# Performance work log

Hardware: AMD Instinct MI355X
Metric: run time of the kernel (lower is better)

## Reference

```python
import jax, jax.numpy as jnp
import numpy as np

B, L, T = 256, 256, 50  # batch, max_len, num_tags


def setup_inputs() -> dict:
    key = jax.random.key(0)
    k1, k2, k3 = jax.random.split(key, 3)
    feats = jax.random.normal(k1, (B, L, T), dtype=jnp.float32)
    trans_m = jax.random.normal(k2, (T, T), dtype=jnp.float32)
    tags = jax.random.randint(k3, (B, L), 0, T)
    mask = jnp.ones((B, L), dtype=jnp.int32)
    return {"feats": feats, "trans_m": trans_m, "tags": tags, "mask": mask}


def _normalizer(logits, trans_m, m):
    # logits: (L, B, T), m: (L, B) float mask
    alpha0 = logits[0]  # (B, T)

    def step(alpha, inp):
        emit, mt = inp  # (B, T), (B,)
        # (B, T_from, T_to) broadcast add, logsumexp over T_from
        tmp = alpha[:, :, None] + trans_m[None, :, :] + emit[:, None, :]
        new = jax.nn.logsumexp(tmp, axis=1)
        alpha = jnp.where(mt[:, None] > 0, new, alpha)
        return alpha, None

    alpha, _ = jax.lax.scan(step, alpha0, (logits[1:], m[1:]))
    return jax.nn.logsumexp(alpha, axis=1)  # (B,)


def _gold_score(logits, trans_m, tags_t, m):
    # logits: (L, B, T); tags_t: (L, B); m: (L, B)
    trans_sc = trans_m[tags_t[:-1], tags_t[1:]] * m[1:]  # (L-1, B)
    emit_sc = jnp.take_along_axis(logits, tags_t[:, :, None], axis=2)[..., 0] * m  # (L, B)
    return jnp.sum(trans_sc + emit_sc[:-1], axis=0) + emit_sc[-1]  # (B,)


def reference(feats, trans_m, tags, mask):
    # feats: (B, L, T) -> (L, B, T); include_start_end_trans=False
    logits = jnp.transpose(feats, (1, 0, 2))
    tags_t = tags.T
    m = mask.T.astype(feats.dtype)
    all_path = _normalizer(logits, trans_m, m)
    gold = _gold_score(logits, trans_m, tags_t, m)
    return all_path - gold  # (B,) loss per example
```

## Files before the change

### kernel.cpp

```cpp
#include <hip/hip_runtime.h>
#include <math.h>


#define TAGS 50
#define LEN 256
#define NB 256
#define HALF 128
#define INV_LN2 1.4426950408889634f
#define LN2 0.6931471805599453f

typedef __attribute__((ext_vector_type(8))) short bf16x8;
typedef __attribute__((ext_vector_type(4))) float f32x4;

#if __has_builtin(__builtin_amdgcn_exp2f)
#define EXP2F(x) __builtin_amdgcn_exp2f(x)
#else
#define EXP2F(x) exp2f(x)
#endif
#if __has_builtin(__builtin_amdgcn_logf)
#define LOG2F(x) __builtin_amdgcn_logf(x)
#else
#define LOG2F(x) log2f(x)
#endif
#if __has_builtin(__builtin_amdgcn_rcpf)
#define RCPF(x) __builtin_amdgcn_rcpf(x)
#else
#define RCPF(x) (1.0f / (x))
#endif

__device__ __forceinline__ float readlane_f(float v, int srclane) {
  return __builtin_bit_cast(float,
      __builtin_amdgcn_readlane(__builtin_bit_cast(int, v), srclane));
}

__device__ __forceinline__ int bf16pair(float lo, float hi) {
  unsigned lb = (__builtin_bit_cast(unsigned, lo) + 0x8000u) >> 16;
  unsigned hb = (__builtin_bit_cast(unsigned, hi) + 0x8000u) & 0xFFFF0000u;
  return (int)(hb | lb);
}

union U8 { int i[4]; bf16x8 v; };

#define WS_U(b)  ((b) * 64)
#define WS_W(b)  ((NB + (b)) * 64)
#define WS_SF(b) (2 * NB * 64 + (b))
#define WS_SB(b) (2 * NB * 64 + NB + (b))

__global__ __launch_bounds__(64) void crf_scan_kernel(
    const float* __restrict__ feats,
    const float* __restrict__ trans,
    const int*   __restrict__ mask,
    float*       __restrict__ ws)
{
  const int bid    = blockIdx.x;
  const bool is_fwd = bid < NB;
  const int b      = is_fwd ? bid : bid - NB;
  const int lane   = threadIdx.x;
  const int q      = lane >> 4;
  const int n      = lane & 15;

  __shared__ __align__(16) float fl[HALF * TAGS];
  __shared__ int ml[HALF];

  const int base_l = is_fwd ? 0 : HALF;
  const float* fb = feats + ((size_t)b * LEN + base_l) * TAGS;
  const int*   mb = mask + b * LEN + base_l;

  {
    const float4* fv = (const float4*)fb;
    for (int i = lane; i < (HALF * TAGS) / 4; i += 64) {
      float4 v4 = fv[i];
      v4.x *= INV_LN2; v4.y *= INV_LN2; v4.z *= INV_LN2; v4.w *= INV_LN2;
      *(float4*)&fl[i * 4] = v4;
    }
    for (int i = lane; i < HALF; i += 64) ml[i] = mb[i];
  }

  int tcl[4], vld[4];
#pragma unroll
  for (int t = 0; t < 4; ++t) {
    const int tg = n + 16 * t;
    vld[t] = tg < TAGS;
    tcl[t] = vld[t] ? tg : (TAGS - 1);
  }

  U8 Bfr[4][2];
#pragma unroll
  for (int t = 0; t < 4; ++t)
#pragma unroll
    for (int c = 0; c < 2; ++c)
#pragma unroll
      for (int r = 0; r < 4; ++r) {
        const int col = 16 * t + n;
        const int tag0 = 16 * c + 4 * q + r;
        const int tag1 = tag0 + 32;
        float e0 = 0.0f, e1 = 0.0f;
        if (col < TAGS) {
          if (tag0 < TAGS)
            e0 = EXP2F((is_fwd ? trans[tag0 * TAGS + col]
                               : trans[col * TAGS + tag0]) * INV_LN2);
          if (tag1 < TAGS)
            e1 = EXP2F((is_fwd ? trans[tag1 * TAGS + col]
                               : trans[col * TAGS + tag1]) * INV_LN2);
        }
        Bfr[t][c].i[r] = bf16pair(e0, e1);
      }

  int addr[4];
#pragma unroll
  for (int r = 0; r < 4; ++r) addr[r] = (4 * q + r) * 4;

  __syncthreads();

  const f32x4 zero4 = {0.0f, 0.0f, 0.0f, 0.0f};
  float v[4], S;

  if (is_fwd) {
    const float c0 = fl[0];
#pragma unroll
    for (int t = 0; t < 4; ++t) v[t] = vld[t] ? EXP2F(fl[tcl[t]] - c0) : 0.0f;
    S = c0;

    float eh[4];
#pragma unroll
    for (int t = 0; t < 4; ++t) eh[t] = EXP2F(fl[TAGS + tcl[t]]);
    int m_nxt = ml[1];

    for (int l = 1; l < HALF; ++l) {
      const int m_cur = m_nxt;
      const int ln = (l + 1 < HALF) ? (l + 1) : (HALF - 1);

      const int P0 = bf16pair(v[0], v[2]);
      const int P1 = bf16pair(v[1], v[3]);
      const float cc = readlane_f(v[0], 0);
      const float rr = RCPF(cc);

      U8 A0, A1;
#pragma unroll
      for (int r = 0; r < 4; ++r) {
        A0.i[r] = __builtin_amdgcn_ds_bpermute(addr[r], P0);
        A1.i[r] = __builtin_amdgcn_ds_bpermute(addr[r], P1);
      }

      f32x4 d0 = __builtin_amdgcn_mfma_f32_16x16x32_bf16(A0.v, Bfr[0][0].v, zero4, 0, 0, 0);
      f32x4 d1 = __builtin_amdgcn_mfma_f32_16x16x32_bf16(A0.v, Bfr[1][0].v, zero4, 0, 0, 0);
      f32x4 d2 = __builtin_amdgcn_mfma_f32_16x16x32_bf16(A0.v, Bfr[2][0].v, zero4, 0, 0, 0);
      f32x4 d3 = __builtin_amdgcn_mfma_f32_16x16x32_bf16(A0.v, Bfr[3][0].v, zero4, 0, 0, 0);
      f32x4 g0 = __builtin_amdgcn_mfma_f32_16x16x32_bf16(A1.v, Bfr[0][1].v, zero4, 0, 0, 0);
      f32x4 g1 = __builtin_amdgcn_mfma_f32_16x16x32_bf16(A1.v, Bfr[1][1].v, zero4, 0, 0, 0);
      f32x4 g2 = __builtin_amdgcn_mfma_f32_16x16x32_bf16(A1.v, Bfr[2][1].v, zero4, 0, 0, 0);
      f32x4 g3 = __builtin_amdgcn_mfma_f32_16x16x32_bf16(A1.v, Bfr[3][1].v, zero4, 0, 0, 0);

      float ehn[4];
#pragma unroll
      for (int t = 0; t < 4; ++t) ehn[t] = fl[ln * TAGS + tcl[t]];
      const int m_n2 = ml[ln];

      v[0] = ((m_cur > 0) ? (d0[0] + g0[0]) * eh[0] : v[0]) * rr;
      v[1] = ((m_cur > 0) ? (d1[0] + g1[0]) * eh[1] : v[1]) * rr;
      v[2] = ((m_cur > 0) ? (d2[0] + g2[0]) * eh[2] : v[2]) * rr;
      v[3] = ((m_cur > 0) ? (d3[0] + g3[0]) * eh[3] : v[3]) * rr;
      S += LOG2F(cc);
#pragma unroll
      for (int t = 0; t < 4; ++t) eh[t] = EXP2F(ehn[t]);
      m_nxt = m_n2;
    }

    if (lane < 16) {
#pragma unroll
      for (int t = 0; t < 4; ++t) ws[WS_U(b) + n + 16 * t] = v[t];
    }
    if (lane == 0) ws[WS_SF(b)] = S;
  } else {
#pragma unroll
    for (int t = 0; t < 4; ++t) v[t] = vld[t] ? 1.0f : 0.0f;
    S = 0.0f;

    float eh[4];
#pragma unroll
    for (int t = 0; t < 4; ++t) eh[t] = EXP2F(fl[(HALF - 1) * TAGS + tcl[t]]);
    int m_nxt = ml[HALF - 1];

    for (int l = HALF - 1; l >= 0; --l) {
      const int m_cur = m_nxt;
      const int ln = (l > 0) ? (l - 1) : 0;

      const float x0 = v[0] * eh[0];
      const float x1 = v[1] * eh[1];
      const float x2 = v[2] * eh[2];
      const float x3 = v[3] * eh[3];
      const int P0 = bf16pair(x0, x2);
      const int P1 = bf16pair(x1, x3);
      const float cc = readlane_f(v[0], 0);
      const float rr = RCPF(cc);

      U8 A0, A1;
#pragma unroll
      for (int r = 0; r < 4; ++r) {
        A0.i[r] = __builtin_amdgcn_ds_bpermute(addr[r], P0);
        A1.i[r] = __builtin_amdgcn_ds_bpermute(addr[r], P1);
      }

      f32x4 d0 = __builtin_amdgcn_mfma_f32_16x16x32_bf16(A0.v, Bfr[0][0].v, zero4, 0, 0, 0);
      f32x4 d1 = __builtin_amdgcn_mfma_f32_16x16x32_bf16(A0.v, Bfr[1][0].v, zero4, 0, 0, 0);
      f32x4 d2 = __builtin_amdgcn_mfma_f32_16x16x32_bf16(A0.v, Bfr[2][0].v, zero4, 0, 0, 0);
      f32x4 d3 = __builtin_amdgcn_mfma_f32_16x16x32_bf16(A0.v, Bfr[3][0].v, zero4, 0, 0, 0);
      f32x4 g0 = __builtin_amdgcn_mfma_f32_16x16x32_bf16(A1.v, Bfr[0][1].v, zero4, 0, 0, 0);
      f32x4 g1 = __builtin_amdgcn_mfma_f32_16x16x32_bf16(A1.v, Bfr[1][1].v, zero4, 0, 0, 0);
      f32x4 g2 = __builtin_amdgcn_mfma_f32_16x16x32_bf16(A1.v, Bfr[2][1].v, zero4, 0, 0, 0);
      f32x4 g3 = __builtin_amdgcn_mfma_f32_16x16x32_bf16(A1.v, Bfr[3][1].v, zero4, 0, 0, 0);

      float ehn[4];
#pragma unroll
      for (int t = 0; t < 4; ++t) ehn[t] = fl[ln * TAGS + tcl[t]];
      const int m_n2 = ml[ln];

      v[0] = ((m_cur > 0) ? (d0[0] + g0[0]) : v[0]) * rr;
      v[1] = ((m_cur > 0) ? (d1[0] + g1[0]) : v[1]) * rr;
      v[2] = ((m_cur > 0) ? (d2[0] + g2[0]) : v[2]) * rr;
      v[3] = ((m_cur > 0) ? (d3[0] + g3[0]) : v[3]) * rr;
      S += LOG2F(cc);
#pragma unroll
      for (int t = 0; t < 4; ++t) eh[t] = EXP2F(ehn[t]);
      m_nxt = m_n2;
    }

    if (lane < 16) {
#pragma unroll
      for (int t = 0; t < 4; ++t) ws[WS_W(b) + n + 16 * t] = v[t];
    }
    if (lane == 0) ws[WS_SB(b)] = S;
  }
}

__global__ __launch_bounds__(64) void crf_combine_kernel(
    const float* __restrict__ feats,
    const float* __restrict__ trans,
    const int*   __restrict__ tags,
    const int*   __restrict__ mask,
    const float* __restrict__ ws,
    float*       __restrict__ out)
{
  const int b = blockIdx.x;
  const int lane = threadIdx.x;

  float s = ws[WS_U(b) + lane] * ws[WS_W(b) + lane];
#pragma unroll
  for (int off = 32; off; off >>= 1) s += __shfl_xor(s, off, 64);

  const float* fb = feats + (size_t)b * (LEN * TAGS);
  const int*   tb = tags + b * LEN;
  const int*   mb = mask + b * LEN;
  float gp = 0.0f;
#pragma unroll
  for (int k = 0; k < 4; ++k) {
    const int p = lane + 64 * k;
    const int tg = tb[p];
    if (mb[p] > 0) {
      float vv = fb[p * TAGS + tg];
      if (p >= 1) vv += trans[tb[p - 1] * TAGS + tg];
      gp += vv;
    }
  }
#pragma unroll
  for (int off = 32; off; off >>= 1) gp += __shfl_xor(gp, off, 64);

  if (lane == 0) {
    const float Sf = ws[WS_SF(b)];
    const float Sb = ws[WS_SB(b)];
    out[b] = LN2 * (Sf + Sb + LOG2F(s)) - gp;
  }
}

extern "C" void kernel_launch(void* const* d_in, const int* in_sizes, int n_in,
                              void* d_out, int out_size, void* d_ws, size_t ws_size,
                              hipStream_t stream) {
  const float* feats = (const float*)d_in[0];
  const float* trans = (const float*)d_in[1];
  const int*   tags  = (const int*)d_in[2];
  const int*   mask  = (const int*)d_in[3];
  float* out = (float*)d_out;
  float* ws  = (float*)d_ws;

  crf_scan_kernel<<<2 * NB, 64, 0, stream>>>(feats, trans, mask, ws);
  crf_combine_kernel<<<NB, 64, 0, stream>>>(feats, trans, tags, mask, ws, out);
}
```

Baseline: 103.9 us.

## Split sequence into chunks with parallel transfer-matrix products combined afterwards

The sequential forward/backward halves shrink from 128 steps each to 32. The 192 middle steps are split into 6 chunks, and separate blocks compute a 64x64 transfer-matrix product for each chunk with MFMA. The combine kernel chains the chunk matrices as matrix-vector products before the final dot product. This shortens the serial dependency chain per block at the cost of much more MFMA work per step, 6x more blocks, and a large workspace of chunk matrices written and reread. A perm-based bf16 pack replaces the shift/mask pack.

```diff
diff --git a/kernel.cpp b/kernel.cpp
--- a/kernel.cpp
+++ b/kernel.cpp
@@ -5,7 +5,9 @@
 #define TAGS 50
 #define LEN 256
 #define NB 256
-#define HALF 128
+#define VST 32
+#define NCH 6
+#define CST 32
 #define INV_LN2 1.4426950408889634f
 #define LN2 0.6931471805599453f
 
@@ -33,18 +35,24 @@
       __builtin_amdgcn_readlane(__builtin_bit_cast(int, v), srclane));
 }
 
-__device__ __forceinline__ int bf16pair(float lo, float hi) {
-  unsigned lb = (__builtin_bit_cast(unsigned, lo) + 0x8000u) >> 16;
-  unsigned hb = (__builtin_bit_cast(unsigned, hi) + 0x8000u) & 0xFFFF0000u;
-  return (int)(hb | lb);
+__device__ __forceinline__ int bfpack(float lo, float hi) {
+  unsigned lb = __builtin_bit_cast(unsigned, lo) + 0x8000u;
+  unsigned hb = __builtin_bit_cast(unsigned, hi) + 0x8000u;
+#if __has_builtin(__builtin_amdgcn_perm)
+  return (int)__builtin_amdgcn_perm(hb, lb, 0x07060302u);
+#else
+  return (int)((hb & 0xFFFF0000u) | (lb >> 16));
+#endif
 }
 
 union U8 { int i[4]; bf16x8 v; };
 
-#define WS_U(b)  ((b) * 64)
-#define WS_W(b)  ((NB + (b)) * 64)
-#define WS_SF(b) (2 * NB * 64 + (b))
-#define WS_SB(b) (2 * NB * 64 + NB + (b))
+#define WS_U(b)    ((b) * 64)
+#define WS_W(b)    ((NB + (b)) * 64)
+#define WS_SF(b)   (2 * NB * 64 + (b))
+#define WS_SB(b)   (2 * NB * 64 + NB + (b))
+#define WS_SC(b,c) (2 * NB * 64 + 2 * NB + (b) * NCH + (c))
+#define WS_T(b,c)  (2 * NB * 64 + 2 * NB + NB * NCH + (((b) * NCH + (c)) * 64) * 64)
 
 __global__ __launch_bounds__(64) void crf_scan_kernel(
     const float* __restrict__ feats,
@@ -52,184 +60,280 @@
     const int*   __restrict__ mask,
     float*       __restrict__ ws)
 {
-  const int bid    = blockIdx.x;
-  const bool is_fwd = bid < NB;
-  const int b      = is_fwd ? bid : bid - NB;
-  const int lane   = threadIdx.x;
-  const int q      = lane >> 4;
-  const int n      = lane & 15;
-
-  __shared__ __align__(16) float fl[HALF * TAGS];
-  __shared__ int ml[HALF];
-
-  const int base_l = is_fwd ? 0 : HALF;
-  const float* fb = feats + ((size_t)b * LEN + base_l) * TAGS;
-  const int*   mb = mask + b * LEN + base_l;
+  const int bid  = blockIdx.x;
+  const int lane = threadIdx.x;
+  const int q    = lane >> 4;
+  const int n    = lane & 15;
+  const f32x4 zero4 = {0.0f, 0.0f, 0.0f, 0.0f};
+
+  if (bid < 2 * NB) {
+    const bool is_fwd = bid < NB;
+    const int b = is_fwd ? bid : bid - NB;
+
+    __shared__ __align__(16) float fl[VST * TAGS];
+    __shared__ int ml[VST];
+
+    const int base_l = is_fwd ? 0 : (LEN - VST);
+    const float* fb = feats + ((size_t)b * LEN + base_l) * TAGS;
+    const int*   mb = mask + b * LEN + base_l;
+
+    {
+      const float4* fv = (const float4*)fb;
+      for (int i = lane; i < (VST * TAGS) / 4; i += 64) {
+        float4 v4 = fv[i];
+        v4.x *= INV_LN2; v4.y *= INV_LN2; v4.z *= INV_LN2; v4.w *= INV_LN2;
+        *(float4*)&fl[i * 4] = v4;
+      }
+      for (int i = lane; i < VST; i += 64) ml[i] = mb[i];
+    }
+
+    int tcl[4], vld[4];
+#pragma unroll
+    for (int t = 0; t < 4; ++t) {
+      const int tg = n + 16 * t;
+      vld[t] = tg < TAGS;
+      tcl[t] = vld[t] ? tg : (TAGS - 1);
+    }
+
+    U8 Bfr[4][2];
+#pragma unroll
+    for (int t = 0; t < 4; ++t)
+#pragma unroll
+      for (int c = 0; c < 2; ++c)
+#pragma unroll
+        for (int r = 0; r < 4; ++r) {
+          const int col = 16 * t + n;
+          const int tag0 = 16 * c + 4 * q + r;
+          const int tag1 = tag0 + 32;
+          float e0 = 0.0f, e1 = 0.0f;
+          if (col < TAGS) {
+            if (tag0 < TAGS)
+              e0 = EXP2F((is_fwd ? trans[tag0 * TAGS + col]
+                                 : trans[col * TAGS + tag0]) * INV_LN2);
+            if (tag1 < TAGS)
+              e1 = EXP2F((is_fwd ? trans[tag1 * TAGS + col]
+                                 : trans[col * TAGS + tag1]) * INV_LN2);
+          }
+          Bfr[t][c].i[r] = bfpack(e0, e1);
+        }
+
+    int addr[4];
+#pragma unroll
+    for (int r = 0; r < 4; ++r) addr[r] = (4 * q + r) * 4;
+
+    __syncthreads();
+
+    float v[4], S;
+    if (is_fwd) {
+      const float c0 = fl[0];
+#pragma unroll
+      for (int t = 0; t < 4; ++t) v[t] = vld[t] ? EXP2F(fl[tcl[t]] - c0) : 0.0f;
+      S = c0;
+      float eh[4];
+#pragma unroll
+      for (int t = 0; t < 4; ++t) eh[t] = EXP2F(fl[TAGS + tcl[t]]);
+      int m_nxt = ml[1];
+
+      for (int l = 1; l < VST; ++l) {
+        const int m_cur = m_nxt;
+        const int ln = (l + 1 < VST) ? (l + 1) : (VST - 1);
+        const int P0 = bfpack(v[0], v[2]);
+        const int P1 = bfpack(v[1], v[3]);
+        const float cc = readlane_f(v[0], 0);
+        const float rr = RCPF(cc);
+        U8 A0, A1;
+#pragma unroll
+        for (int r = 0; r < 4; ++r) {
+          A0.i[r] = __builtin_amdgcn_ds_bpermute(addr[r], P0);
+          A1.i[r] = __builtin_amdgcn_ds_bpermute(addr[r], P1);
+        }
+        f32x4 d0 = __builtin_amdgcn_mfma_f32_16x16x32_bf16(A0.v, Bfr[0][0].v, zero4, 0, 0, 0);
+        f32x4 d1 = __builtin_amdgcn_mfma_f32_16x16x32_bf16(A0.v, Bfr[1][0].v, zero4, 0, 0, 0);
+        f32x4 d2 = __builtin_amdgcn_mfma_f32_16x16x32_bf16(A0.v, Bfr[2][0].v, zero4, 0, 0, 0);
+        f32x4 d3 = __builtin_amdgcn_mfma_f32_16x16x32_bf16(A0.v, Bfr[3][0].v, zero4, 0, 0, 0);
+        f32x4 g0 = __builtin_amdgcn_mfma_f32_16x16x32_bf16(A1.v, Bfr[0][1].v, zero4, 0, 0, 0);
+        f32x4 g1 = __builtin_amdgcn_mfma_f32_16x16x32_bf16(A1.v, Bfr[1][1].v, zero4, 0, 0, 0);
+        f32x4 g2 = __builtin_amdgcn_mfma_f32_16x16x32_bf16(A1.v, Bfr[2][1].v, zero4, 0, 0, 0);
+        f32x4 g3 = __builtin_amdgcn_mfma_f32_16x16x32_bf16(A1.v, Bfr[3][1].v, zero4, 0, 0, 0);
+        float ehn[4];
+#pragma unroll
+        for (int t = 0; t < 4; ++t) ehn[t] = fl[ln * TAGS + tcl[t]];
+        const int m_n2 = ml[ln];
+        v[0] = ((m_cur > 0) ? (d0[0] + g0[0]) * eh[0] : v[0]) * rr;
+        v[1] = ((m_cur > 0) ? (d1[0] + g1[0]) * eh[1] : v[1]) * rr;
+        v[2] = ((m_cur > 0) ? (d2[0] + g2[0]) * eh[2] : v[2]) * rr;
+        v[3] = ((m_cur > 0) ? (d3[0] + g3[0]) * eh[3] : v[3]) * rr;
+        S += LOG2F(cc);
+#pragma unroll
+        for (int t = 0; t < 4; ++t) eh[t] = EXP2F(ehn[t]);
+        m_nxt = m_n2;
+      }
+      if (lane < 16) {
+#pragma unroll
+        for (int t = 0; t < 4; ++t) ws[WS_U(b) + n + 16 * t] = v[t];
+      }
+      if (lane == 0) ws[WS_SF(b)] = S;
+    } else {
+#pragma unroll
+      for (int t = 0; t < 4; ++t) v[t] = vld[t] ? 1.0f : 0.0f;
+      S = 0.0f;
+      float eh[4];
+#pragma unroll
+      for (int t = 0; t < 4; ++t) eh[t] = EXP2F(fl[(VST - 1) * TAGS + tcl[t]]);
+      int m_nxt = ml[VST - 1];
+
+      for (int l = VST - 1; l >= 0; --l) {
+        const int m_cur = m_nxt;
+        const int ln = (l > 0) ? (l - 1) : 0;
+        const float x0 = v[0] * eh[0];
+        const float x1 = v[1] * eh[1];
+        const float x2 = v[2] * eh[2];
+        const float x3 = v[3] * eh[3];
+        const int P0 = bfpack(x0, x2);
+        const int P1 = bfpack(x1, x3);
+        const float cc = readlane_f(v[0], 0);
+        const float rr = RCPF(cc);
+        U8 A0, A1;
+#pragma unroll
+        for (int r = 0; r < 4; ++r) {
+          A0.i[r] = __builtin_amdgcn_ds_bpermute(addr[r], P0);
+          A1.i[r] = __builtin_amdgcn_ds_bpermute(addr[r], P1);
+        }
+        f32x4 d0 = __builtin_amdgcn_mfma_f32_16x16x32_bf16(A0.v, Bfr[0][0].v, zero4, 0, 0, 0);
+        f32x4 d1 = __builtin_amdgcn_mfma_f32_16x16x32_bf16(A0.v, Bfr[1][0].v, zero4, 0, 0, 0);
+        f32x4 d2 = __builtin_amdgcn_mfma_f32_16x16x32_bf16(A0.v, Bfr[2][0].v, zero4, 0, 0, 0);
+        f32x4 d3 = __builtin_amdgcn_mfma_f32_16x16x32_bf16(A0.v, Bfr[3][0].v, zero4, 0, 0, 0);
+        f32x4 g0 = __builtin_amdgcn_mfma_f32_16x16x32_bf16(A1.v, Bfr[0][1].v, zero4, 0, 0, 0);
+        f32x4 g1 = __builtin_amdgcn_mfma_f32_16x16x32_bf16(A1.v, Bfr[1][1].v, zero4, 0, 0, 0);
+        f32x4 g2 = __builtin_amdgcn_mfma_f32_16x16x32_bf16(A1.v, Bfr[2][1].v, zero4, 0, 0, 0);
+        f32x4 g3 = __builtin_amdgcn_mfma_f32_16x16x32_bf16(A1.v, Bfr[3][1].v, zero4, 0, 0, 0);
+        float ehn[4];
+#pragma unroll
+        for (int t = 0; t < 4; ++t) ehn[t] = fl[ln * TAGS + tcl[t]];
+        const int m_n2 = ml[ln];
+        v[0] = ((m_cur > 0) ? (d0[0] + g0[0]) : v[0]) * rr;
+        v[1] = ((m_cur > 0) ? (d1[0] + g1[0]) : v[1]) * rr;
+        v[2] = ((m_cur > 0) ? (d2[0] + g2[0]) : v[2]) * rr;
+        v[3] = ((m_cur > 0) ? (d3[0] + g3[0]) : v[3]) * rr;
+        S += LOG2F(cc);
+#pragma unroll
+        for (int t = 0; t < 4; ++t) eh[t] = EXP2F(ehn[t]);
+        m_nxt = m_n2;
+      }
+      if (lane < 16) {
+#pragma unroll
+        for (int t = 0; t < 4; ++t) ws[WS_W(b) + n + 16 * t] = v[t];
+      }
+      if (lane == 0) ws[WS_SB(b)] = S;
+    }
+    return;
+  }
 
   {
-    const float4* fv = (const float4*)fb;
-    for (int i = lane; i < (HALF * TAGS) / 4; i += 64) {
-      float4 v4 = fv[i];
-      v4.x *= INV_LN2; v4.y *= INV_LN2; v4.z *= INV_LN2; v4.w *= INV_LN2;
-      *(float4*)&fl[i * 4] = v4;
-    }
-    for (int i = lane; i < HALF; i += 64) ml[i] = mb[i];
-  }
-
-  int tcl[4], vld[4];
-#pragma unroll
-  for (int t = 0; t < 4; ++t) {
-    const int tg = n + 16 * t;
-    vld[t] = tg < TAGS;
-    tcl[t] = vld[t] ? tg : (TAGS - 1);
-  }
-
-  U8 Bfr[4][2];
-#pragma unroll
-  for (int t = 0; t < 4; ++t)
-#pragma unroll
-    for (int c = 0; c < 2; ++c)
-#pragma unroll
-      for (int r = 0; r < 4; ++r) {
-        const int col = 16 * t + n;
-        const int tag0 = 16 * c + 4 * q + r;
-        const int tag1 = tag0 + 32;
-        float e0 = 0.0f, e1 = 0.0f;
-        if (col < TAGS) {
-          if (tag0 < TAGS)
-            e0 = EXP2F((is_fwd ? trans[tag0 * TAGS + col]
-                               : trans[col * TAGS + tag0]) * INV_LN2);
-          if (tag1 < TAGS)
-            e1 = EXP2F((is_fwd ? trans[tag1 * TAGS + col]
-                               : trans[col * TAGS + tag1]) * INV_LN2);
-        }
-        Bfr[t][c].i[r] = bf16pair(e0, e1);
-      }
-
-  int addr[4];
-#pragma unroll
-  for (int r = 0; r < 4; ++r) addr[r] = (4 * q + r) * 4;
-
-  __syncthreads();
-
-  const f32x4 zero4 = {0.0f, 0.0f, 0.0f, 0.0f};
-  float v[4], S;
-
-  if (is_fwd) {
-    const float c0 = fl[0];
-#pragma unroll
-    for (int t = 0; t < 4; ++t) v[t] = vld[t] ? EXP2F(fl[tcl[t]] - c0) : 0.0f;
-    S = c0;
-
-    float eh[4];
-#pragma unroll
-    for (int t = 0; t < 4; ++t) eh[t] = EXP2F(fl[TAGS + tcl[t]]);
-    int m_nxt = ml[1];
-
-    for (int l = 1; l < HALF; ++l) {
-      const int m_cur = m_nxt;
-      const int ln = (l + 1 < HALF) ? (l + 1) : (HALF - 1);
-
-      const int P0 = bf16pair(v[0], v[2]);
-      const int P1 = bf16pair(v[1], v[3]);
-      const float cc = readlane_f(v[0], 0);
-      const float rr = RCPF(cc);
-
-      U8 A0, A1;
-#pragma unroll
-      for (int r = 0; r < 4; ++r) {
-        A0.i[r] = __builtin_amdgcn_ds_bpermute(addr[r], P0);
-        A1.i[r] = __builtin_amdgcn_ds_bpermute(addr[r], P1);
-      }
-
-      f32x4 d0 = __builtin_amdgcn_mfma_f32_16x16x32_bf16(A0.v, Bfr[0][0].v, zero4, 0, 0, 0);
-      f32x4 d1 = __builtin_amdgcn_mfma_f32_16x16x32_bf16(A0.v, Bfr[1][0].v, zero4, 0, 0, 0);
-      f32x4 d2 = __builtin_amdgcn_mfma_f32_16x16x32_bf16(A0.v, Bfr[2][0].v, zero4, 0, 0, 0);
-      f32x4 d3 = __builtin_amdgcn_mfma_f32_16x16x32_bf16(A0.v, Bfr[3][0].v, zero4, 0, 0, 0);
-      f32x4 g0 = __builtin_amdgcn_mfma_f32_16x16x32_bf16(A1.v, Bfr[0][1].v, zero4, 0, 0, 0);
-      f32x4 g1 = __builtin_amdgcn_mfma_f32_16x16x32_bf16(A1.v, Bfr[1][1].v, zero4, 0, 0, 0);
-      f32x4 g2 = __builtin_amdgcn_mfma_f32_16x16x32_bf16(A1.v, Bfr[2][1].v, zero4, 0, 0, 0);
-      f32x4 g3 = __builtin_amdgcn_mfma_f32_16x16x32_bf16(A1.v, Bfr[3][1].v, zero4, 0, 0, 0);
-
-      float ehn[4];
-#pragma unroll
-      for (int t = 0; t < 4; ++t) ehn[t] = fl[ln * TAGS + tcl[t]];
-      const int m_n2 = ml[ln];
-
-      v[0] = ((m_cur > 0) ? (d0[0] + g0[0]) * eh[0] : v[0]) * rr;
-      v[1] = ((m_cur > 0) ? (d1[0] + g1[0]) * eh[1] : v[1]) * rr;
-      v[2] = ((m_cur > 0) ? (d2[0] + g2[0]) * eh[2] : v[2]) * rr;
-      v[3] = ((m_cur > 0) ? (d3[0] + g3[0]) * eh[3] : v[3]) * rr;
-      S += LOG2F(cc);
-#pragma unroll
-      for (int t = 0; t < 4; ++t) eh[t] = EXP2F(ehn[t]);
-      m_nxt = m_n2;
-    }
-
-    if (lane < 16) {
-#pragma unroll
-      for (int t = 0; t < 4; ++t) ws[WS_U(b) + n + 16 * t] = v[t];
-    }
-    if (lane == 0) ws[WS_SF(b)] = S;
-  } else {
-#pragma unroll
-    for (int t = 0; t < 4; ++t) v[t] = vld[t] ? 1.0f : 0.0f;
-    S = 0.0f;
-
-    float eh[4];
-#pragma unroll
-    for (int t = 0; t < 4; ++t) eh[t] = EXP2F(fl[(HALF - 1) * TAGS + tcl[t]]);
-    int m_nxt = ml[HALF - 1];
-
-    for (int l = HALF - 1; l >= 0; --l) {
-      const int m_cur = m_nxt;
-      const int ln = (l > 0) ? (l - 1) : 0;
-
-      const float x0 = v[0] * eh[0];
-      const float x1 = v[1] * eh[1];
-      const float x2 = v[2] * eh[2];
-      const float x3 = v[3] * eh[3];
-      const int P0 = bf16pair(x0, x2);
-      const int P1 = bf16pair(x1, x3);
-      const float cc = readlane_f(v[0], 0);
-      const float rr = RCPF(cc);
-
-      U8 A0, A1;
-#pragma unroll
-      for (int r = 0; r < 4; ++r) {
-        A0.i[r] = __builtin_amdgcn_ds_bpermute(addr[r], P0);
-        A1.i[r] = __builtin_amdgcn_ds_bpermute(addr[r], P1);
-      }
-
-      f32x4 d0 = __builtin_amdgcn_mfma_f32_16x16x32_bf16(A0.v, Bfr[0][0].v, zero4, 0, 0, 0);
-      f32x4 d1 = __builtin_amdgcn_mfma_f32_16x16x32_bf16(A0.v, Bfr[1][0].v, zero4, 0, 0, 0);
-      f32x4 d2 = __builtin_amdgcn_mfma_f32_16x16x32_bf16(A0.v, Bfr[2][0].v, zero4, 0, 0, 0);
-      f32x4 d3 = __builtin_amdgcn_mfma_f32_16x16x32_bf16(A0.v, Bfr[3][0].v, zero4, 0, 0, 0);
-      f32x4 g0 = __builtin_amdgcn_mfma_f32_16x16x32_bf16(A1.v, Bfr[0][1].v, zero4, 0, 0, 0);
-      f32x4 g1 = __builtin_amdgcn_mfma_f32_16x16x32_bf16(A1.v, Bfr[1][1].v, zero4, 0, 0, 0);
-      f32x4 g2 = __builtin_amdgcn_mfma_f32_16x16x32_bf16(A1.v, Bfr[2][1].v, zero4, 0, 0, 0);
-      f32x4 g3 = __builtin_amdgcn_mfma_f32_16x16x32_bf16(A1.v, Bfr[3][1].v, zero4, 0, 0, 0);
-
-      float ehn[4];
-#pragma unroll
-      for (int t = 0; t < 4; ++t) ehn[t] = fl[ln * TAGS + tcl[t]];
-      const int m_n2 = ml[ln];
-
-      v[0] = ((m_cur > 0) ? (d0[0] + g0[0]) : v[0]) * rr;
-      v[1] = ((m_cur > 0) ? (d1[0] + g1[0]) : v[1]) * rr;
-      v[2] = ((m_cur > 0) ? (d2[0] + g2[0]) : v[2]) * rr;
-      v[3] = ((m_cur > 0) ? (d3[0] + g3[0]) : v[3]) * rr;
-      S += LOG2F(cc);
-#pragma unroll
-      for (int t = 0; t < 4; ++t) eh[t] = EXP2F(ehn[t]);
-      m_nxt = m_n2;
-    }
-
-    if (lane < 16) {
-#pragma unroll
-      for (int t = 0; t < 4; ++t) ws[WS_W(b) + n + 16 * t] = v[t];
-    }
-    if (lane == 0) ws[WS_SB(b)] = S;
+    const int i2 = bid - 2 * NB;
+    const int b = i2 / NCH;
+    const int cidx = i2 - b * NCH;
+    const int l0 = CST * (cidx + 1);
+
+    __shared__ __align__(16) float em[CST * 52 + 16];
+    __shared__ int ml[CST];
+
+    for (int i = lane; i < CST * 52 + 16; i += 64) em[i] = 0.0f;
+    __syncthreads();
+
+    const float* fbc = feats + ((size_t)b * LEN + l0) * TAGS;
+    {
+      const float4* fv = (const float4*)fbc;
+      for (int i = lane; i < (CST * TAGS) / 4; i += 64) {
+        const float4 v4 = fv[i];
+        const int g = i * 4;
+#pragma unroll
+        for (int e = 0; e < 4; ++e) {
+          const int gg = g + e;
+          const int row = gg / TAGS;
+          const int col = gg - row * TAGS;
+          const float val = (e == 0) ? v4.x : (e == 1) ? v4.y : (e == 2) ? v4.z : v4.w;
+          em[row * 52 + col] = val * INV_LN2;
+        }
+      }
+      for (int i = lane; i < CST; i += 64) ml[i] = mask[b * LEN + l0 + i];
+    }
+
+    U8 Afr[4][2];
+#pragma unroll
+    for (int tm = 0; tm < 4; ++tm)
+#pragma unroll
+      for (int c2 = 0; c2 < 2; ++c2)
+#pragma unroll
+        for (int rr = 0; rr < 4; ++rr) {
+          const int m = 16 * tm + n;
+          const int kr = 32 * c2 + 16 * (rr >> 1) + 4 * q + 2 * (rr & 1);
+          const float e0 = (m < TAGS && kr < TAGS)
+              ? EXP2F(trans[kr * TAGS + m] * INV_LN2) : 0.0f;
+          const float e1 = (m < TAGS && kr + 1 < TAGS)
+              ? EXP2F(trans[(kr + 1) * TAGS + m] * INV_LN2) : 0.0f;
+          Afr[tm][c2].i[rr] = bfpack(e0, e1);
+        }
+
+    __syncthreads();
+
+    f32x4 d[4][4];
+#pragma unroll
+    for (int tm = 0; tm < 4; ++tm)
+#pragma unroll
+      for (int tn = 0; tn < 4; ++tn)
+#pragma unroll
+        for (int e = 0; e < 4; ++e)
+          d[tm][tn][e] = (tm == tn && n == 4 * q + e) ? 1.0f : 0.0f;
+
+    float S = 0.0f;
+
+    for (int l = 0; l < CST; ++l) {
+      if (ml[l] > 0) {
+        const float cc = readlane_f(d[0][0][0], 0);
+        const float rv = RCPF(cc);
+
+        U8 Bf[2][4];
+#pragma unroll
+        for (int c2 = 0; c2 < 2; ++c2)
+#pragma unroll
+          for (int tn = 0; tn < 4; ++tn) {
+            Bf[c2][tn].i[0] = bfpack(d[2 * c2][tn][0], d[2 * c2][tn][1]);
+            Bf[c2][tn].i[1] = bfpack(d[2 * c2][tn][2], d[2 * c2][tn][3]);
+            Bf[c2][tn].i[2] = bfpack(d[2 * c2 + 1][tn][0], d[2 * c2 + 1][tn][1]);
+            Bf[c2][tn].i[3] = bfpack(d[2 * c2 + 1][tn][2], d[2 * c2 + 1][tn][3]);
+          }
+
+        float sc[4][4];
+#pragma unroll
+        for (int tm = 0; tm < 4; ++tm) {
+          const f32x4 er = *(const f32x4*)&em[l * 52 + 16 * tm + 4 * q];
+#pragma unroll
+          for (int e = 0; e < 4; ++e) sc[tm][e] = EXP2F(er[e]) * rv;
+        }
+
+#pragma unroll
+        for (int tm = 0; tm < 4; ++tm)
+#pragma unroll
+          for (int tn = 0; tn < 4; ++tn) {
+            f32x4 acc = __builtin_amdgcn_mfma_f32_16x16x32_bf16(
+                Afr[tm][0].v, Bf[0][tn].v, zero4, 0, 0, 0);
+            acc = __builtin_amdgcn_mfma_f32_16x16x32_bf16(
+                Afr[tm][1].v, Bf[1][tn].v, acc, 0, 0, 0);
+#pragma unroll
+            for (int e = 0; e < 4; ++e) d[tm][tn][e] = acc[e] * sc[tm][e];
+          }
+        S += LOG2F(cc);
+      }
+    }
+
+    float* tw = ws + WS_T(b, cidx) + lane * 64;
+#pragma unroll
+    for (int tm = 0; tm < 4; ++tm)
+#pragma unroll
+      for (int tn = 0; tn < 4; ++tn)
+        *(f32x4*)&tw[(tm * 4 + tn) * 4] = d[tm][tn];
+    if (lane == 0) ws[WS_SC(b, cidx)] = S;
   }
 }
 
@@ -244,7 +348,27 @@
   const int b = blockIdx.x;
   const int lane = threadIdx.x;
 
-  float s = ws[WS_U(b) + lane] * ws[WS_W(b) + lane];
+  float x = ws[WS_U(b) + lane];
+  float Ssum = 0.0f;
+
+  const int rbase = ((lane & 15) >> 2) * 16 * 64 + (lane >> 4) * 16 + (lane & 3);
+  for (int c = 0; c < NCH; ++c) {
+    const float* Tb = ws + WS_T(b, c) + rbase;
+    float a0 = 0.0f, a1 = 0.0f, a2 = 0.0f, a3 = 0.0f;
+#pragma unroll
+    for (int i = 0; i < 64; i += 4) {
+      a0 = fmaf(Tb[((i + 0) & 15) * 64 + ((i + 0) >> 4) * 4], readlane_f(x, i + 0), a0);
+      a1 = fmaf(Tb[((i + 1) & 15) * 64 + ((i + 1) >> 4) * 4], readlane_f(x, i + 1), a1);
+      a2 = fmaf(Tb[((i + 2) & 15) * 64 + ((i + 2) >> 4) * 4], readlane_f(x, i + 2), a2);
+      a3 = fmaf(Tb[((i + 3) & 15) * 64 + ((i + 3) >> 4) * 4], readlane_f(x, i + 3), a3);
+    }
+    const float acc = (a0 + a1) + (a2 + a3);
+    const float cc = readlane_f(acc, 0);
+    x = acc * RCPF(cc);
+    Ssum += LOG2F(cc) + ws[WS_SC(b, c)];
+  }
+
+  float s = x * ws[WS_W(b) + lane];
 #pragma unroll
   for (int off = 32; off; off >>= 1) s += __shfl_xor(s, off, 64);
 
@@ -268,7 +392,7 @@
   if (lane == 0) {
     const float Sf = ws[WS_SF(b)];
     const float Sb = ws[WS_SB(b)];
-    out[b] = LN2 * (Sf + Sb + LOG2F(s)) - gp;
+    out[b] = LN2 * (Sf + Sb + Ssum + LOG2F(s)) - gp;
   }
 }
 
@@ -282,6 +406,6 @@
   float* out = (float*)d_out;
   float* ws  = (float*)d_ws;
 
-  crf_scan_kernel<<<2 * NB, 64, 0, stream>>>(feats, trans, mask, ws);
+  crf_scan_kernel<<<2 * NB + NB * NCH, 64, 0, stream>>>(feats, trans, mask, ws);
   crf_combine_kernel<<<NB, 64, 0, stream>>>(feats, trans, tags, mask, ws, out);
 }
```

Measured after the change: 128.2 us. 1.23x slower.
